# Kernel optimization log

Hardware: AMD Instinct MI355X
Metric: run time of the kernel (lower is better)

Reference implementation:

```python
import jax, jax.numpy as jnp
import numpy as np

DEFAULT_MASK_VALUE = -0.7 * float(np.finfo(np.float32).max)

B, S, HQ, HKV, D = 2, 2048, 16, 8, 128
CHUNK = 512


def _chunk_causal_mask(seq_len, chunk_size):
    # True where attention allowed: same chunk AND causal within chunk.
    row = jax.lax.broadcasted_iota(jnp.int32, (seq_len, seq_len), 0)
    col = jax.lax.broadcasted_iota(jnp.int32, (seq_len, seq_len), 1)
    return (row // chunk_size == col // chunk_size) & (row >= col)


def _block_mask_indices(bidirectional_mask):
    # [B, L] 0/1 -> segment ids, e.g. [0,1,1,1,0,0,1,1,0,1,0] -> [0,1,1,1,0,0,2,2,0,3,0]
    m = bidirectional_mask.astype(jnp.int32)
    padded = jnp.pad(m, [(0, 0), (1, 0)], constant_values=0)
    boundary = padded[..., 1:] > padded[..., :-1]
    return m * jnp.cumsum(boundary, axis=-1)


def _bidirectional_block_mask(bidirectional_mask):
    idx = _block_mask_indices(bidirectional_mask)  # [B, L]
    return (idx[:, None, :] == idx[:, :, None]) & (idx[:, :, None] > 0)  # [B, L, L]


def setup_inputs() -> dict:
    key = jax.random.key(0)
    kq, kk, kv, kb = jax.random.split(key, 4)
    q = jax.random.normal(kq, (B, S, HQ, D), dtype=jnp.float32)
    k = jax.random.normal(kk, (B, S, HKV, D), dtype=jnp.float32)
    v = jax.random.normal(kv, (B, S, HKV, D), dtype=jnp.float32)
    bidirectional_mask = jax.random.randint(kb, (B, S), 0, 2, dtype=jnp.int32)
    return {"q": q, "k": k, "v": v, "bidirectional_mask": bidirectional_mask,
            "chunk_size": CHUNK}


def reference(q, k, v, bidirectional_mask, chunk_size):
    b, s, hq, d = q.shape
    hkv = k.shape[2]
    group = hq // hkv  # GQA group size
    scale = 1.0 / jnp.sqrt(jnp.asarray(d, q.dtype))

    # [b, s, hkv, group, d]
    qg = q.reshape(b, s, hkv, group, d) * scale
    # logits: [b, hkv, group, q, kv]
    logits = jnp.einsum("bqhgd,bkhd->bhgqk", qg, k)

    # combined mask: chunked-causal OR bidirectional block (image tokens attend
    # bidirectionally within their contiguous block)
    chunk_mask = _chunk_causal_mask(s, chunk_size)                 # [s, s]
    bidir_mask = _bidirectional_block_mask(bidirectional_mask)    # [b, s, s]
    allowed = chunk_mask[None, :, :] | bidir_mask                  # [b, s, s]
    allowed = allowed[:, None, None, :, :]                         # [b, 1, 1, s, s]

    masked = jnp.where(allowed, logits, DEFAULT_MASK_VALUE)
    probs = jax.nn.softmax(masked, axis=-1)

    out = jnp.einsum("bhgqk,bkhd->bqhgd", probs, v)
    return out.reshape(b, s, hq, d)
```

## Files before the change

### kernel.cpp

```cpp
#include <hip/hip_runtime.h>
#include <hip/hip_bf16.h>

#define SLEN 2048
#define BATCH 2
#define NHQ 16
#define NHKV 8
#define DIM 128
#define SEG 512
#define NSEG (SLEN / SEG)
#define KVROW (NHKV * DIM)

#define KTD (64 * 64)
#define VTD (128 * 32)
#define PLSD (16 * 32)

typedef __attribute__((ext_vector_type(8))) short bf16x8;
typedef __attribute__((ext_vector_type(4))) float f32x4;

static __device__ inline short f2bf(float f) {
    __hip_bfloat16 h = __float2bfloat16(f);
    return *reinterpret_cast<short*>(&h);
}
static __device__ inline unsigned pack_bf2(float lo, float hi) {
    unsigned a = (unsigned)(unsigned short)f2bf(lo);
    unsigned b = (unsigned)(unsigned short)f2bf(hi);
    return a | (b << 16);
}
static __device__ inline float fast_exp2(float x) {
#if __has_builtin(__builtin_amdgcn_exp2f)
    return __builtin_amdgcn_exp2f(x);
#else
    return __builtin_exp2f(x);
#endif
}

#define GLDS(g, l) __builtin_amdgcn_global_load_lds( \
    (const __attribute__((address_space(1))) void*)(g), \
    (__attribute__((address_space(3))) void*)(l), 16, 0, 0)

__global__ __launch_bounds__(256) void conv_kv(
    const float* __restrict__ K, const float* __restrict__ V,
    unsigned short* __restrict__ Kb, unsigned short* __restrict__ Vt,
    const int* __restrict__ mask, int* __restrict__ rs, int* __restrict__ re)
{
    __shared__ float vt_s[64 * 132];
    __shared__ int   sm[SLEN];
    const int blk = blockIdx.x;
    const int NCONV = BATCH * NHKV * (SLEN / 64);

    if (blk >= NCONV) {
        const int idx = blk - NCONV;
        const int b = idx >> 3, slice = idx & 7;
        const int* mb = mask + b * SLEN;
        for (int i = threadIdx.x; i < SLEN; i += 256) sm[i] = mb[i];
        __syncthreads();
        const int i = slice * 256 + threadIdx.x;
        int s0 = -1, e0 = -2;
        if (sm[i] == 1) {
            s0 = i; while (s0 > 0 && sm[s0 - 1] == 1) --s0;
            e0 = i; while (e0 < SLEN - 1 && sm[e0 + 1] == 1) ++e0;
        }
        rs[b * SLEN + i] = s0;
        re[b * SLEN + i] = e0;
        return;
    }

    const int st = blk & 31;
    const int h  = (blk >> 5) & 7;
    const int b  = blk >> 8;
    const int s0 = st * 64;
    const int sl = threadIdx.x >> 2;
    const int dq = (threadIdx.x & 3) * 32;

    {
        const float* ksrc = K + (((size_t)(b * SLEN + s0 + sl) * NHKV + h) * DIM) + dq;
        unsigned short* kdst = Kb + (((size_t)(b * NHKV + h) * SLEN) + s0 + sl) * DIM + dq;
        #pragma unroll
        for (int i = 0; i < 4; ++i) {
            float4 a = ((const float4*)ksrc)[2 * i];
            float4 c = ((const float4*)ksrc)[2 * i + 1];
            ((uint4*)kdst)[i] = make_uint4(pack_bf2(a.x, a.y), pack_bf2(a.z, a.w),
                                           pack_bf2(c.x, c.y), pack_bf2(c.z, c.w));
        }
    }

    {
        const float* vsrc = V + (((size_t)(b * SLEN + s0 + sl) * NHKV + h) * DIM) + dq;
        float4* ld = (float4*)&vt_s[sl * 132 + dq];
        #pragma unroll
        for (int i = 0; i < 8; ++i) ld[i] = ((const float4*)vsrc)[i];
    }
    __syncthreads();
    #pragma unroll
    for (int pass = 0; pass < 2; ++pass) {
        const int dl = (threadIdx.x >> 2) + pass * 64;
        const int sw = (threadIdx.x & 3) * 16;
        unsigned pk[8];
        #pragma unroll
        for (int m = 0; m < 8; ++m)
            pk[m] = pack_bf2(vt_s[(sw + 2 * m) * 132 + dl],
                             vt_s[(sw + 2 * m + 1) * 132 + dl]);
        unsigned short* dst = Vt + (((size_t)(b * NHKV + h) * DIM) + dl) * SLEN + s0 + sw;
        ((uint4*)dst)[0] = make_uint4(pk[0], pk[1], pk[2], pk[3]);
        ((uint4*)dst)[1] = make_uint4(pk[4], pk[5], pk[6], pk[7]);
    }
}

__global__ __launch_bounds__(512, 2) void attn_fwd(
    const float* __restrict__ Q, const unsigned short* __restrict__ KbP,
    const unsigned short* __restrict__ VtP, const int* __restrict__ rs,
    const int* __restrict__ re, const int* __restrict__ csp,
    float* __restrict__ Out)
{
    const int tid  = threadIdx.x;
    const int wid  = tid >> 6;
    const int lane = tid & 63;
    const int quad = lane >> 4;
    const int n    = lane & 15;

    const int bid = blockIdx.x;
    const int xcd = bid & 7;
    const int M   = (bid >> 3) & 7;
    const int G   = (bid >> 6) * 8 + xcd;
    const int seg = G & 3;
    const int h   = (G >> 2) & 7;
    const int b   = G >> 5;
    const int par = M >> 1;
    const int hq  = h * 2 + (M & 1);

    const int rbase = seg * SEG;
    const int r0 = rbase + (4 * wid + par) * 16;

    __shared__ unsigned pool[2 * KTD + 2 * VTD + 8 * PLSD];
    short* pw = (short*)(pool + 2 * KTD + 2 * VTD) + wid * (16 * 64);

    const float scale = 0.08838834764831845f * 1.4426950408889634f;
    const int cs = csp[0];

    const int* rsb = rs + b * SLEN;
    const int* reb = re + b * SLEN;

    const int row  = r0 + n;
    const int rsvq = rsb[row];
    const int csrq = (row / cs) * cs;
    int lo_rt, hi_rt;
    {
        const int revq = reb[row];
        int lo = csrq; if (rsvq >= 0 && rsvq < lo) lo = rsvq;
        int hi = row;  if (revq > hi) hi = revq;
        #pragma unroll
        for (int off = 8; off > 0; off >>= 1) {
            lo = min(lo, __shfl_xor(lo, off, 64));
            hi = max(hi, __shfl_xor(hi, off, 64));
        }
        lo_rt = lo; hi_rt = hi;
    }
    const int cshi = ((r0 + 15) / cs) * cs;

    bf16x8 qa[4];
    {
        const float* qp = Q + (((size_t)(b * SLEN + row) * NHQ + hq) * DIM) + quad * 8;
        #pragma unroll
        for (int kb = 0; kb < 4; ++kb) {
            float4 f0 = *(const float4*)(qp + kb * 32);
            float4 f1 = *(const float4*)(qp + kb * 32 + 4);
            bf16x8 a;
            a[0] = f2bf(f0.x * scale); a[1] = f2bf(f0.y * scale);
            a[2] = f2bf(f0.z * scale); a[3] = f2bf(f0.w * scale);
            a[4] = f2bf(f1.x * scale); a[5] = f2bf(f1.y * scale);
            a[6] = f2bf(f1.z * scale); a[7] = f2bf(f1.w * scale);
            qa[kb] = a;
        }
    }

    int lo_blk, hi_blk;
    {
        int* sred = (int*)pool;
        if (lane == 0) { sred[wid * 2] = lo_rt; sred[wid * 2 + 1] = hi_rt; }
        __syncthreads();
        int lo = 0x7fffffff, hi = 0;
        #pragma unroll
        for (int i = 0; i < 8; ++i) {
            lo = min(lo, sred[2 * i]);
            hi = max(hi, sred[2 * i + 1]);
        }
        __syncthreads();
        lo_blk = lo & ~63;
        hi_blk = hi;
    }

    float lrow[4] = {0.f, 0.f, 0.f, 0.f};
    f32x4 o[8];
    #pragma unroll
    for (int nb = 0; nb < 8; ++nb) o[nb] = (f32x4){0.f, 0.f, 0.f, 0.f};

    const unsigned short* KbB = KbP + (size_t)(b * NHKV + h) * SLEN * DIM;
    const unsigned short* VtB = VtP + (size_t)(b * NHKV + h) * DIM * SLEN;
    int ks_off[2], vs_off[2];
    unsigned kl_off[2], vl_off[2];
    #pragma unroll
    for (int q2 = 0; q2 < 2; ++q2) {
        const int B = q2 * 512 + tid;
        { const int r = B >> 4, j = B & 15;
          const int sj = (j & 8) | ((j & 7) ^ (r & 7));
          ks_off[q2] = r * DIM + sj * 8;  kl_off[q2] = (unsigned)B * 16; }
        { const int r = B >> 3, j = B & 7;
          const int sj = j ^ (r & 7);
          vs_off[q2] = r * SLEN + sj * 8; vl_off[q2] = (unsigned)B * 16; }
    }

    const unsigned kxr = (unsigned)((n & 7) << 2);

    {
        const unsigned short* kbt = KbB + (size_t)lo_blk * DIM;
        const unsigned short* vtt = VtB + lo_blk;
        char* kl = (char*)pool;
        char* vl = (char*)pool + 32768;
        #pragma unroll
        for (int q2 = 0; q2 < 2; ++q2) {
            GLDS(kbt + ks_off[q2], kl + kl_off[q2]);
            GLDS(vtt + vs_off[q2], vl + vl_off[q2]);
        }
    }
    int rsv_c = rsb[lo_blk + lane];
    __syncthreads();

    int bufi = 0;
    for (int k0 = lo_blk; k0 <= hi_blk; k0 += 64, bufi ^= 1) {
        int rsv_n = rsv_c;
        if (k0 + 64 <= hi_blk) {
            const int kn0 = k0 + 64;
            const unsigned short* kbt = KbB + (size_t)kn0 * DIM;
            const unsigned short* vtt = VtB + kn0;
            char* kl = (char*)pool + (bufi ^ 1) * 16384;
            char* vl = (char*)pool + 32768 + (bufi ^ 1) * 16384;
            #pragma unroll
            for (int q2 = 0; q2 < 2; ++q2) {
                GLDS(kbt + ks_off[q2], kl + kl_off[q2]);
                GLDS(vtt + vs_off[q2], vl + vl_off[q2]);
            }
            rsv_n = rsb[kn0 + lane];
        }

        if ((k0 + 63 >= lo_rt) && (k0 <= hi_rt)) {
            const unsigned* ktb = pool + bufi * KTD;
            const unsigned* vtb = pool + 2 * KTD + bufi * VTD;

            f32x4 sfr[4];
            #pragma unroll
            for (int c = 0; c < 4; ++c) sfr[c] = (f32x4){0.f, 0.f, 0.f, 0.f};
            __builtin_amdgcn_s_setprio(1);
            #pragma unroll
            for (int c = 0; c < 4; ++c) {
                #pragma unroll
                for (int kb = 0; kb < 4; ++kb) {
                    const bf16x8 kf = *(const bf16x8*)(ktb +
                        (((unsigned)((c * 16 + n) * 64 + kb * 16 + quad * 4)) ^ kxr));
                    sfr[c] = __builtin_amdgcn_mfma_f32_16x16x32_bf16(qa[kb], kf, sfr[c], 0, 0, 0);
                }
            }
            __builtin_amdgcn_s_setprio(0);

            const bool fullc = (k0 >= cshi) && (k0 + 63 <= r0);
            if (!fullc) {
                int rsr[4], csr_g[4];
                #pragma unroll
                for (int g = 0; g < 4; ++g) {
                    rsr[g]   = __shfl(rsvq, quad * 4 + g, 64);
                    csr_g[g] = __shfl(csrq, quad * 4 + g, 64);
                }
                #pragma unroll
                for (int c = 0; c < 4; ++c) {
                    const int kcl  = k0 + c * 16 + n;
                    const int rskv = __shfl(rsv_c, c * 16 + n, 64);
                    #pragma unroll
                    for (int g = 0; g < 4; ++g) {
                        const int r = r0 + quad * 4 + g;
                        const bool ok = ((kcl >= csr_g[g]) && (kcl <= r)) ||
                                        (rsr[g] >= 0 && rskv == rsr[g]);
                        if (!ok) sfr[c][g] = -3.0e38f;
                    }
                }
            }

            float psum[4] = {0.f, 0.f, 0.f, 0.f};
            #pragma unroll
            for (int c = 0; c < 4; ++c) {
                #pragma unroll
                for (int g = 0; g < 4; ++g) {
                    const float pv = fast_exp2(sfr[c][g]);
                    psum[g] += pv;
                    const int prow = quad * 4 + g;
                    pw[((unsigned)(prow * 64 + c * 16 + n)) ^ ((unsigned)((prow & 7) << 3))] = f2bf(pv);
                }
            }
            #pragma unroll
            for (int g = 0; g < 4; ++g) lrow[g] += psum[g];

            __builtin_amdgcn_s_setprio(1);
            #pragma unroll
            for (int kb2 = 0; kb2 < 2; ++kb2) {
                const bf16x8 pa = *(const bf16x8*)(pw +
                    (((unsigned)(n * 64 + kb2 * 32 + quad * 8)) ^ ((unsigned)((n & 7) << 3))));
                #pragma unroll
                for (int nb = 0; nb < 8; ++nb) {
                    const bf16x8 vf = *(const bf16x8*)(vtb +
                        (((unsigned)((nb * 16 + n) * 32 + kb2 * 16 + quad * 4)) ^ kxr));
                    o[nb] = __builtin_amdgcn_mfma_f32_16x16x32_bf16(pa, vf, o[nb], 0, 0, 0);
                }
            }
            __builtin_amdgcn_s_setprio(0);
        }

        __syncthreads();
        rsv_c = rsv_n;
    }

    #pragma unroll
    for (int g = 0; g < 4; ++g) {
        float l = lrow[g];
        #pragma unroll
        for (int off = 8; off > 0; off >>= 1)
            l += __shfl_xor(l, off, 64);
        const float inv = 1.0f / l;
        const int r = r0 + quad * 4 + g;
        float* op = Out + ((size_t)(b * SLEN + r) * NHQ + hq) * DIM + n;
        #pragma unroll
        for (int nb = 0; nb < 8; ++nb)
            op[nb * 16] = o[nb][g] * inv;
    }
}

extern "C" void kernel_launch(void* const* d_in, const int* in_sizes, int n_in,
                              void* d_out, int out_size, void* d_ws, size_t ws_size,
                              hipStream_t stream) {
    const float* q  = (const float*)d_in[0];
    const float* k  = (const float*)d_in[1];
    const float* v  = (const float*)d_in[2];
    const int*   bm = (const int*)d_in[3];
    const int*   cs = (const int*)d_in[4];
    float* out = (float*)d_out;

    int* rs = (int*)d_ws;
    int* re = rs + BATCH * SLEN;
    unsigned short* Kb = (unsigned short*)((char*)d_ws + 32768);
    unsigned short* Vt = Kb + (size_t)BATCH * NHKV * SLEN * DIM;

    hipLaunchKernelGGL(conv_kv, dim3(BATCH * NHKV * (SLEN / 64) + BATCH * 8), dim3(256),
                       0, stream, k, v, Kb, Vt, bm, rs, re);
    hipLaunchKernelGGL(attn_fwd, dim3(BATCH * NHQ * NSEG * 4), dim3(512), 0, stream,
                       q, Kb, Vt, rs, re, cs, out);
}
```

Baseline: 150.5 us.

## Drop LDS K/V staging; load fragments directly from global with small blocks

Replaces the 512-thread blocks that double-buffer K and V tiles into shared memory via global_load_lds with 128-thread blocks of two waves. Each wave now reads its K and V MFMA fragments straight from global memory (through L2 and cache) and walks only its own key range. Block-wide min/max reductions and per-iteration barriers go away. Blocks are remapped so heavy rows are scheduled first and XCDs group by batch and head. The cost is no explicit K/V reuse across the waves of a block and unhidden global load latency, which now depends on occupancy and cache hits.

```diff
diff --git a/kernel.cpp b/kernel.cpp
--- a/kernel.cpp
+++ b/kernel.cpp
@@ -8,11 +8,6 @@
 #define DIM 128
 #define SEG 512
 #define NSEG (SLEN / SEG)
-#define KVROW (NHKV * DIM)
-
-#define KTD (64 * 64)
-#define VTD (128 * 32)
-#define PLSD (16 * 32)
 
 typedef __attribute__((ext_vector_type(8))) short bf16x8;
 typedef __attribute__((ext_vector_type(4))) float f32x4;
@@ -33,10 +28,6 @@
     return __builtin_exp2f(x);
 #endif
 }
-
-#define GLDS(g, l) __builtin_amdgcn_global_load_lds( \
-    (const __attribute__((address_space(1))) void*)(g), \
-    (__attribute__((address_space(3))) void*)(l), 16, 0, 0)
 
 __global__ __launch_bounds__(256) void conv_kv(
     const float* __restrict__ K, const float* __restrict__ V,
@@ -106,7 +97,7 @@
     }
 }
 
-__global__ __launch_bounds__(512, 2) void attn_fwd(
+__global__ __launch_bounds__(128, 8) void attn_fwd(
     const float* __restrict__ Q, const unsigned short* __restrict__ KbP,
     const unsigned short* __restrict__ VtP, const int* __restrict__ rs,
     const int* __restrict__ re, const int* __restrict__ csp,
@@ -118,21 +109,23 @@
     const int quad = lane >> 4;
     const int n    = lane & 15;
 
-    const int bid = blockIdx.x;
-    const int xcd = bid & 7;
-    const int M   = (bid >> 3) & 7;
-    const int G   = (bid >> 6) * 8 + xcd;
-    const int seg = G & 3;
-    const int h   = (G >> 2) & 7;
-    const int b   = G >> 5;
-    const int par = M >> 1;
-    const int hq  = h * 2 + (M & 1);
-
-    const int rbase = seg * SEG;
-    const int r0 = rbase + (4 * wid + par) * 16;
-
-    __shared__ unsigned pool[2 * KTD + 2 * VTD + 8 * PLSD];
-    short* pw = (short*)(pool + 2 * KTD + 2 * VTD) + wid * (16 * 64);
+    const int bid    = blockIdx.x;
+    const int xcd    = bid & 7;
+    const int rest   = bid >> 3;
+    const int plocal = rest >> 7;
+    const int inner  = rest & 127;
+    const int bh = xcd * 2 + plocal;
+    const int b  = bh >> 3;
+    const int h  = bh & 7;
+    const int hq = h * 2 + (inner & 1);
+    const int pr = inner >> 1;
+    const int chunk = pr & 3;
+    const int p2 = pr >> 2;
+    const int pos = 31 - (p2 * 2 + wid);
+    const int r0 = chunk * SEG + pos * 16;
+
+    __shared__ short pls[2][16 * 64];
+    short* pw = pls[wid];
 
     const float scale = 0.08838834764831845f * 1.4426950408889634f;
     const int cs = csp[0];
@@ -156,6 +149,13 @@
         lo_rt = lo; hi_rt = hi;
     }
     const int cshi = ((r0 + 15) / cs) * cs;
+
+    int rsr[4], csr_g[4];
+    #pragma unroll
+    for (int g = 0; g < 4; ++g) {
+        rsr[g]   = __shfl(rsvq, quad * 4 + g, 64);
+        csr_g[g] = __shfl(csrq, quad * 4 + g, 64);
+    }
 
     bf16x8 qa[4];
     {
@@ -173,22 +173,6 @@
         }
     }
 
-    int lo_blk, hi_blk;
-    {
-        int* sred = (int*)pool;
-        if (lane == 0) { sred[wid * 2] = lo_rt; sred[wid * 2 + 1] = hi_rt; }
-        __syncthreads();
-        int lo = 0x7fffffff, hi = 0;
-        #pragma unroll
-        for (int i = 0; i < 8; ++i) {
-            lo = min(lo, sred[2 * i]);
-            hi = max(hi, sred[2 * i + 1]);
-        }
-        __syncthreads();
-        lo_blk = lo & ~63;
-        hi_blk = hi;
-    }
-
     float lrow[4] = {0.f, 0.f, 0.f, 0.f};
     f32x4 o[8];
     #pragma unroll
@@ -196,124 +180,72 @@
 
     const unsigned short* KbB = KbP + (size_t)(b * NHKV + h) * SLEN * DIM;
     const unsigned short* VtB = VtP + (size_t)(b * NHKV + h) * DIM * SLEN;
-    int ks_off[2], vs_off[2];
-    unsigned kl_off[2], vl_off[2];
-    #pragma unroll
-    for (int q2 = 0; q2 < 2; ++q2) {
-        const int B = q2 * 512 + tid;
-        { const int r = B >> 4, j = B & 15;
-          const int sj = (j & 8) | ((j & 7) ^ (r & 7));
-          ks_off[q2] = r * DIM + sj * 8;  kl_off[q2] = (unsigned)B * 16; }
-        { const int r = B >> 3, j = B & 7;
-          const int sj = j ^ (r & 7);
-          vs_off[q2] = r * SLEN + sj * 8; vl_off[q2] = (unsigned)B * 16; }
-    }
-
-    const unsigned kxr = (unsigned)((n & 7) << 2);
-
-    {
-        const unsigned short* kbt = KbB + (size_t)lo_blk * DIM;
-        const unsigned short* vtt = VtB + lo_blk;
-        char* kl = (char*)pool;
-        char* vl = (char*)pool + 32768;
-        #pragma unroll
-        for (int q2 = 0; q2 < 2; ++q2) {
-            GLDS(kbt + ks_off[q2], kl + kl_off[q2]);
-            GLDS(vtt + vs_off[q2], vl + vl_off[q2]);
-        }
-    }
-    int rsv_c = rsb[lo_blk + lane];
-    __syncthreads();
-
-    int bufi = 0;
-    for (int k0 = lo_blk; k0 <= hi_blk; k0 += 64, bufi ^= 1) {
-        int rsv_n = rsv_c;
-        if (k0 + 64 <= hi_blk) {
-            const int kn0 = k0 + 64;
-            const unsigned short* kbt = KbB + (size_t)kn0 * DIM;
-            const unsigned short* vtt = VtB + kn0;
-            char* kl = (char*)pool + (bufi ^ 1) * 16384;
-            char* vl = (char*)pool + 32768 + (bufi ^ 1) * 16384;
-            #pragma unroll
-            for (int q2 = 0; q2 < 2; ++q2) {
-                GLDS(kbt + ks_off[q2], kl + kl_off[q2]);
-                GLDS(vtt + vs_off[q2], vl + vl_off[q2]);
-            }
-            rsv_n = rsb[kn0 + lane];
-        }
-
-        if ((k0 + 63 >= lo_rt) && (k0 <= hi_rt)) {
-            const unsigned* ktb = pool + bufi * KTD;
-            const unsigned* vtb = pool + 2 * KTD + bufi * VTD;
-
-            f32x4 sfr[4];
-            #pragma unroll
-            for (int c = 0; c < 4; ++c) sfr[c] = (f32x4){0.f, 0.f, 0.f, 0.f};
-            __builtin_amdgcn_s_setprio(1);
+
+    for (int k0 = (lo_rt & ~63); k0 <= hi_rt; k0 += 64) {
+        const bool fullc = (k0 >= cshi) && (k0 + 63 <= r0);
+
+        int rskv[4];
+        if (!fullc) {
+            #pragma unroll
+            for (int c = 0; c < 4; ++c) rskv[c] = rsb[k0 + c * 16 + n];
+        }
+
+        const unsigned short* kt = KbB + (size_t)k0 * DIM;
+        f32x4 sfr[4];
+        #pragma unroll
+        for (int c = 0; c < 4; ++c) sfr[c] = (f32x4){0.f, 0.f, 0.f, 0.f};
+        __builtin_amdgcn_s_setprio(1);
+        #pragma unroll
+        for (int c = 0; c < 4; ++c) {
+            #pragma unroll
+            for (int kb = 0; kb < 4; ++kb) {
+                const bf16x8 kf = *(const bf16x8*)(kt + (c * 16 + n) * DIM + kb * 32 + quad * 8);
+                sfr[c] = __builtin_amdgcn_mfma_f32_16x16x32_bf16(qa[kb], kf, sfr[c], 0, 0, 0);
+            }
+        }
+        __builtin_amdgcn_s_setprio(0);
+
+        if (!fullc) {
             #pragma unroll
             for (int c = 0; c < 4; ++c) {
-                #pragma unroll
-                for (int kb = 0; kb < 4; ++kb) {
-                    const bf16x8 kf = *(const bf16x8*)(ktb +
-                        (((unsigned)((c * 16 + n) * 64 + kb * 16 + quad * 4)) ^ kxr));
-                    sfr[c] = __builtin_amdgcn_mfma_f32_16x16x32_bf16(qa[kb], kf, sfr[c], 0, 0, 0);
-                }
-            }
-            __builtin_amdgcn_s_setprio(0);
-
-            const bool fullc = (k0 >= cshi) && (k0 + 63 <= r0);
-            if (!fullc) {
-                int rsr[4], csr_g[4];
+                const int kcl = k0 + c * 16 + n;
                 #pragma unroll
                 for (int g = 0; g < 4; ++g) {
-                    rsr[g]   = __shfl(rsvq, quad * 4 + g, 64);
-                    csr_g[g] = __shfl(csrq, quad * 4 + g, 64);
+                    const int r = r0 + quad * 4 + g;
+                    const bool ok = ((kcl >= csr_g[g]) && (kcl <= r)) ||
+                                    (rsr[g] >= 0 && rskv[c] == rsr[g]);
+                    if (!ok) sfr[c][g] = -3.0e38f;
                 }
-                #pragma unroll
-                for (int c = 0; c < 4; ++c) {
-                    const int kcl  = k0 + c * 16 + n;
-                    const int rskv = __shfl(rsv_c, c * 16 + n, 64);
-                    #pragma unroll
-                    for (int g = 0; g < 4; ++g) {
-                        const int r = r0 + quad * 4 + g;
-                        const bool ok = ((kcl >= csr_g[g]) && (kcl <= r)) ||
-                                        (rsr[g] >= 0 && rskv == rsr[g]);
-                        if (!ok) sfr[c][g] = -3.0e38f;
-                    }
-                }
-            }
-
-            float psum[4] = {0.f, 0.f, 0.f, 0.f};
-            #pragma unroll
-            for (int c = 0; c < 4; ++c) {
-                #pragma unroll
-                for (int g = 0; g < 4; ++g) {
-                    const float pv = fast_exp2(sfr[c][g]);
-                    psum[g] += pv;
-                    const int prow = quad * 4 + g;
-                    pw[((unsigned)(prow * 64 + c * 16 + n)) ^ ((unsigned)((prow & 7) << 3))] = f2bf(pv);
-                }
-            }
-            #pragma unroll
-            for (int g = 0; g < 4; ++g) lrow[g] += psum[g];
-
-            __builtin_amdgcn_s_setprio(1);
-            #pragma unroll
-            for (int kb2 = 0; kb2 < 2; ++kb2) {
-                const bf16x8 pa = *(const bf16x8*)(pw +
-                    (((unsigned)(n * 64 + kb2 * 32 + quad * 8)) ^ ((unsigned)((n & 7) << 3))));
-                #pragma unroll
-                for (int nb = 0; nb < 8; ++nb) {
-                    const bf16x8 vf = *(const bf16x8*)(vtb +
-                        (((unsigned)((nb * 16 + n) * 32 + kb2 * 16 + quad * 4)) ^ kxr));
-                    o[nb] = __builtin_amdgcn_mfma_f32_16x16x32_bf16(pa, vf, o[nb], 0, 0, 0);
-                }
-            }
-            __builtin_amdgcn_s_setprio(0);
-        }
-
-        __syncthreads();
-        rsv_c = rsv_n;
+            }
+        }
+
+        float psum[4] = {0.f, 0.f, 0.f, 0.f};
+        #pragma unroll
+        for (int c = 0; c < 4; ++c) {
+            #pragma unroll
+            for (int g = 0; g < 4; ++g) {
+                const float pv = fast_exp2(sfr[c][g]);
+                psum[g] += pv;
+                const int prow = quad * 4 + g;
+                pw[((unsigned)(prow * 64 + c * 16 + n)) ^ ((unsigned)((prow & 7) << 3))] = f2bf(pv);
+            }
+        }
+        #pragma unroll
+        for (int g = 0; g < 4; ++g) lrow[g] += psum[g];
+
+        const unsigned short* vt = VtB + k0;
+        __builtin_amdgcn_s_setprio(1);
+        #pragma unroll
+        for (int kb2 = 0; kb2 < 2; ++kb2) {
+            const bf16x8 pa = *(const bf16x8*)(pw +
+                (((unsigned)(n * 64 + kb2 * 32 + quad * 8)) ^ ((unsigned)((n & 7) << 3))));
+            #pragma unroll
+            for (int nb = 0; nb < 8; ++nb) {
+                const bf16x8 vf = *(const bf16x8*)(vt + (size_t)(nb * 16 + n) * SLEN + kb2 * 32 + quad * 8);
+                o[nb] = __builtin_amdgcn_mfma_f32_16x16x32_bf16(pa, vf, o[nb], 0, 0, 0);
+            }
+        }
+        __builtin_amdgcn_s_setprio(0);
     }
 
     #pragma unroll
@@ -348,6 +280,6 @@
 
     hipLaunchKernelGGL(conv_kv, dim3(BATCH * NHKV * (SLEN / 64) + BATCH * 8), dim3(256),
                        0, stream, k, v, Kb, Vt, bm, rs, re);
-    hipLaunchKernelGGL(attn_fwd, dim3(BATCH * NHQ * NSEG * 4), dim3(512), 0, stream,
+    hipLaunchKernelGGL(attn_fwd, dim3(2048), dim3(128), 0, stream,
                        q, Kb, Vt, rs, re, cs, out);
 }
```

After: 285.3 us. 1.9x slower.

## Keep P in registers via transposed QK^T and 16x16x16 MFMA for PV

Applied to the files above, without the earlier changes.

The QK^T MFMA operands are swapped so each lane holds scores for one query row across four key columns. Those scores are exponentiated and packed straight into bf16x4 operands for 16x16x16 MFMAs over V, which removes the LDS round trip for P and its per-warp scratch buffer. The block-to-tile mapping is also changed to row bands ordered heaviest first, and the K/V swizzle and load addressing are simplified. The risk is lower throughput from the smaller-K MFMA, and the unverified new swizzle or the inline-asm fallback could give wrong results.

```diff
diff --git a/kernel.cpp b/kernel.cpp
--- a/kernel.cpp
+++ b/kernel.cpp
@@ -8,13 +8,12 @@
 #define DIM 128
 #define SEG 512
 #define NSEG (SLEN / SEG)
-#define KVROW (NHKV * DIM)
 
 #define KTD (64 * 64)
 #define VTD (128 * 32)
-#define PLSD (16 * 32)
 
 typedef __attribute__((ext_vector_type(8))) short bf16x8;
+typedef __attribute__((ext_vector_type(4))) short bf16x4;
 typedef __attribute__((ext_vector_type(4))) float f32x4;
 
 static __device__ inline short f2bf(float f) {
@@ -31,6 +30,15 @@
     return __builtin_amdgcn_exp2f(x);
 #else
     return __builtin_exp2f(x);
+#endif
+}
+static __device__ inline f32x4 mfma16(bf16x4 a, bf16x4 b, f32x4 c) {
+#if __has_builtin(__builtin_amdgcn_mfma_f32_16x16x16bf16_1k)
+    return __builtin_amdgcn_mfma_f32_16x16x16bf16_1k(a, b, c, 0, 0, 0);
+#else
+    asm volatile("v_mfma_f32_16x16x16_bf16 %0, %1, %2, %0\n\ts_nop 7\n\ts_nop 7"
+                 : "+v"(c) : "v"(a), "v"(b));
+    return c;
 #endif
 }
 
@@ -118,21 +126,17 @@
     const int quad = lane >> 4;
     const int n    = lane & 15;
 
-    const int bid = blockIdx.x;
-    const int xcd = bid & 7;
-    const int M   = (bid >> 3) & 7;
-    const int G   = (bid >> 6) * 8 + xcd;
-    const int seg = G & 3;
-    const int h   = (G >> 2) & 7;
-    const int b   = G >> 5;
-    const int par = M >> 1;
-    const int hq  = h * 2 + (M & 1);
-
-    const int rbase = seg * SEG;
-    const int r0 = rbase + (4 * wid + par) * 16;
-
-    __shared__ unsigned pool[2 * KTD + 2 * VTD + 8 * PLSD];
-    short* pw = (short*)(pool + 2 * KTD + 2 * VTD) + wid * (16 * 64);
+    const int bid   = blockIdx.x;
+    const int h     = bid & 7;
+    const int inner = (bid >> 3) & 15;
+    const int q4    = (bid >> 7) & 3;
+    const int band  = (q4 == 0) ? 3 : (q4 == 1) ? 2 : (q4 == 2) ? 0 : 1;
+    const int b     = inner & 1;
+    const int hq    = h * 2 + ((inner >> 1) & 1);
+    const int chunk = inner >> 2;
+    const int r0 = chunk * SEG + band * 128 + wid * 16;
+
+    __shared__ unsigned pool[2 * KTD + 2 * VTD];
 
     const float scale = 0.08838834764831845f * 1.4426950408889634f;
     const int cs = csp[0];
@@ -189,40 +193,33 @@
         hi_blk = hi;
     }
 
-    float lrow[4] = {0.f, 0.f, 0.f, 0.f};
+    float lrow = 0.0f;
     f32x4 o[8];
     #pragma unroll
     for (int nb = 0; nb < 8; ++nb) o[nb] = (f32x4){0.f, 0.f, 0.f, 0.f};
 
     const unsigned short* KbB = KbP + (size_t)(b * NHKV + h) * SLEN * DIM;
     const unsigned short* VtB = VtP + (size_t)(b * NHKV + h) * DIM * SLEN;
-    int ks_off[2], vs_off[2];
-    unsigned kl_off[2], vl_off[2];
-    #pragma unroll
-    for (int q2 = 0; q2 < 2; ++q2) {
-        const int B = q2 * 512 + tid;
-        { const int r = B >> 4, j = B & 15;
-          const int sj = (j & 8) | ((j & 7) ^ (r & 7));
-          ks_off[q2] = r * DIM + sj * 8;  kl_off[q2] = (unsigned)B * 16; }
-        { const int r = B >> 3, j = B & 7;
-          const int sj = j ^ (r & 7);
-          vs_off[q2] = r * SLEN + sj * 8; vl_off[q2] = (unsigned)B * 16; }
-    }
-
-    const unsigned kxr = (unsigned)((n & 7) << 2);
-
-    {
-        const unsigned short* kbt = KbB + (size_t)lo_blk * DIM;
-        const unsigned short* vtt = VtB + lo_blk;
+
+    const int kr0  = tid >> 4;
+    const int ksl  = (tid & 15) ^ (kr0 & 15);
+    const size_t koff = (size_t)kr0 * DIM + ksl * 8;
+    const int vr0  = tid >> 3;
+    const int vsl  = (tid & 7) ^ (vr0 & 7);
+    const size_t voff = (size_t)vr0 * SLEN + vsl * 8;
+
+    int rsv_c;
+    {
+        const unsigned short* ks = KbB + (size_t)lo_blk * DIM + koff;
+        const unsigned short* vs = VtB + lo_blk + voff;
         char* kl = (char*)pool;
         char* vl = (char*)pool + 32768;
-        #pragma unroll
-        for (int q2 = 0; q2 < 2; ++q2) {
-            GLDS(kbt + ks_off[q2], kl + kl_off[q2]);
-            GLDS(vtt + vs_off[q2], vl + vl_off[q2]);
-        }
-    }
-    int rsv_c = rsb[lo_blk + lane];
+        GLDS(ks,                     kl + tid * 16);
+        GLDS(ks + (size_t)32 * DIM,  kl + 8192 + tid * 16);
+        GLDS(vs,                     vl + tid * 16);
+        GLDS(vs + (size_t)64 * SLEN, vl + 8192 + tid * 16);
+        rsv_c = rsb[lo_blk + lane];
+    }
     __syncthreads();
 
     int bufi = 0;
@@ -230,21 +227,20 @@
         int rsv_n = rsv_c;
         if (k0 + 64 <= hi_blk) {
             const int kn0 = k0 + 64;
-            const unsigned short* kbt = KbB + (size_t)kn0 * DIM;
-            const unsigned short* vtt = VtB + kn0;
+            const unsigned short* ks = KbB + (size_t)kn0 * DIM + koff;
+            const unsigned short* vs = VtB + kn0 + voff;
             char* kl = (char*)pool + (bufi ^ 1) * 16384;
             char* vl = (char*)pool + 32768 + (bufi ^ 1) * 16384;
-            #pragma unroll
-            for (int q2 = 0; q2 < 2; ++q2) {
-                GLDS(kbt + ks_off[q2], kl + kl_off[q2]);
-                GLDS(vtt + vs_off[q2], vl + vl_off[q2]);
-            }
+            GLDS(ks,                     kl + tid * 16);
+            GLDS(ks + (size_t)32 * DIM,  kl + 8192 + tid * 16);
+            GLDS(vs,                     vl + tid * 16);
+            GLDS(vs + (size_t)64 * SLEN, vl + 8192 + tid * 16);
             rsv_n = rsb[kn0 + lane];
         }
 
         if ((k0 + 63 >= lo_rt) && (k0 <= hi_rt)) {
-            const unsigned* ktb = pool + bufi * KTD;
-            const unsigned* vtb = pool + 2 * KTD + bufi * VTD;
+            const short* ktb = (const short*)(pool + bufi * KTD);
+            const short* vtb = (const short*)(pool + 2 * KTD + bufi * VTD);
 
             f32x4 sfr[4];
             #pragma unroll
@@ -255,58 +251,48 @@
                 #pragma unroll
                 for (int kb = 0; kb < 4; ++kb) {
                     const bf16x8 kf = *(const bf16x8*)(ktb +
-                        (((unsigned)((c * 16 + n) * 64 + kb * 16 + quad * 4)) ^ kxr));
-                    sfr[c] = __builtin_amdgcn_mfma_f32_16x16x32_bf16(qa[kb], kf, sfr[c], 0, 0, 0);
+                        (c * 16 + n) * DIM + (((kb * 4 + quad) ^ n) * 8));
+                    sfr[c] = __builtin_amdgcn_mfma_f32_16x16x32_bf16(kf, qa[kb], sfr[c], 0, 0, 0);
                 }
             }
             __builtin_amdgcn_s_setprio(0);
 
             const bool fullc = (k0 >= cshi) && (k0 + 63 <= r0);
             if (!fullc) {
-                int rsr[4], csr_g[4];
-                #pragma unroll
-                for (int g = 0; g < 4; ++g) {
-                    rsr[g]   = __shfl(rsvq, quad * 4 + g, 64);
-                    csr_g[g] = __shfl(csrq, quad * 4 + g, 64);
-                }
                 #pragma unroll
                 for (int c = 0; c < 4; ++c) {
-                    const int kcl  = k0 + c * 16 + n;
-                    const int rskv = __shfl(rsv_c, c * 16 + n, 64);
                     #pragma unroll
                     for (int g = 0; g < 4; ++g) {
-                        const int r = r0 + quad * 4 + g;
-                        const bool ok = ((kcl >= csr_g[g]) && (kcl <= r)) ||
-                                        (rsr[g] >= 0 && rskv == rsr[g]);
+                        const int kcl  = k0 + c * 16 + quad * 4 + g;
+                        const int rskv = __shfl(rsv_c, c * 16 + quad * 4 + g, 64);
+                        const bool ok = ((kcl >= csrq) && (kcl <= row)) ||
+                                        (rsvq >= 0 && rskv == rsvq);
                         if (!ok) sfr[c][g] = -3.0e38f;
                     }
                 }
             }
 
-            float psum[4] = {0.f, 0.f, 0.f, 0.f};
+            bf16x4 pa[4];
+            #pragma unroll
+            for (int c = 0; c < 4; ++c) {
+                float p0 = fast_exp2(sfr[c][0]);
+                float p1 = fast_exp2(sfr[c][1]);
+                float p2 = fast_exp2(sfr[c][2]);
+                float p3 = fast_exp2(sfr[c][3]);
+                lrow += (p0 + p1) + (p2 + p3);
+                uint2 ww = make_uint2(pack_bf2(p0, p1), pack_bf2(p2, p3));
+                pa[c] = __builtin_bit_cast(bf16x4, ww);
+            }
+
+            __builtin_amdgcn_s_setprio(1);
             #pragma unroll
             for (int c = 0; c < 4; ++c) {
                 #pragma unroll
-                for (int g = 0; g < 4; ++g) {
-                    const float pv = fast_exp2(sfr[c][g]);
-                    psum[g] += pv;
-                    const int prow = quad * 4 + g;
-                    pw[((unsigned)(prow * 64 + c * 16 + n)) ^ ((unsigned)((prow & 7) << 3))] = f2bf(pv);
-                }
-            }
-            #pragma unroll
-            for (int g = 0; g < 4; ++g) lrow[g] += psum[g];
-
-            __builtin_amdgcn_s_setprio(1);
-            #pragma unroll
-            for (int kb2 = 0; kb2 < 2; ++kb2) {
-                const bf16x8 pa = *(const bf16x8*)(pw +
-                    (((unsigned)(n * 64 + kb2 * 32 + quad * 8)) ^ ((unsigned)((n & 7) << 3))));
-                #pragma unroll
                 for (int nb = 0; nb < 8; ++nb) {
-                    const bf16x8 vf = *(const bf16x8*)(vtb +
-                        (((unsigned)((nb * 16 + n) * 32 + kb2 * 16 + quad * 4)) ^ kxr));
-                    o[nb] = __builtin_amdgcn_mfma_f32_16x16x32_bf16(pa, vf, o[nb], 0, 0, 0);
+                    const bf16x4 vb = *(const bf16x4*)(vtb +
+                        (nb * 16 + n) * 64 + (((c * 2 + (quad >> 1)) ^ (n & 7)) * 8)
+                        + (quad & 1) * 4);
+                    o[nb] = mfma16(pa[c], vb, o[nb]);
                 }
             }
             __builtin_amdgcn_s_setprio(0);
@@ -316,18 +302,17 @@
         rsv_c = rsv_n;
     }
 
+    lrow += __shfl_xor(lrow, 16, 64);
+    lrow += __shfl_xor(lrow, 32, 64);
+    const float inv = 1.0f / lrow;
     #pragma unroll
     for (int g = 0; g < 4; ++g) {
-        float l = lrow[g];
-        #pragma unroll
-        for (int off = 8; off > 0; off >>= 1)
-            l += __shfl_xor(l, off, 64);
-        const float inv = 1.0f / l;
+        const float invg = __shfl(inv, quad * 4 + g, 64);
         const int r = r0 + quad * 4 + g;
         float* op = Out + ((size_t)(b * SLEN + r) * NHQ + hq) * DIM + n;
         #pragma unroll
         for (int nb = 0; nb < 8; ++nb)
-            op[nb * 16] = o[nb][g] * inv;
+            op[nb * 16] = o[nb][g] * invg;
     }
 }
 
@@ -348,6 +333,6 @@
 
     hipLaunchKernelGGL(conv_kv, dim3(BATCH * NHKV * (SLEN / 64) + BATCH * 8), dim3(256),
                        0, stream, k, v, Kb, Vt, bm, rs, re);
-    hipLaunchKernelGGL(attn_fwd, dim3(BATCH * NHQ * NSEG * 4), dim3(512), 0, stream,
+    hipLaunchKernelGGL(attn_fwd, dim3(512), dim3(512), 0, stream,
                        q, Kb, Vt, rs, re, cs, out);
 }
```

Measured after the change: 131.3 us. -12.7%, faster.
